# Optimization experiments

Hardware: AMD Instinct MI355X
Metric: run time of the kernel (lower is better)

Reference implementation:

```python
import jax, jax.numpy as jnp
import numpy as np

DIST_W = 1.0
LOGIT_W = 1.0


def _lsa(cost):
    """Rectangular linear sum assignment (Jonker-Volgenant shortest augmenting
    path), numpy-vectorized inner loop. cost: (n, m) with n <= m.
    Returns (row_ind, col_ind) matching scipy.optimize.linear_sum_assignment."""
    cost = np.asarray(cost, dtype=np.float64)
    n, m = cost.shape
    assert n <= m
    INF = 1e18
    u = np.zeros(n + 1)
    v = np.zeros(m + 1)
    p = np.zeros(m + 1, dtype=np.int64)   # p[j] = row matched to col j (1-based), 0 = free
    way = np.zeros(m + 1, dtype=np.int64)
    for i in range(1, n + 1):
        p[0] = i
        j0 = 0
        minv = np.full(m + 1, INF)
        used = np.zeros(m + 1, dtype=bool)
        while True:
            used[j0] = True
            i0 = p[j0]
            js = np.nonzero(~used[1:])[0] + 1          # free columns (1-based)
            cur = cost[i0 - 1, js - 1] - u[i0] - v[js]
            better = cur < minv[js]
            minv[js] = np.where(better, cur, minv[js])
            way[js[better]] = j0
            k = int(np.argmin(minv[js]))
            delta = minv[js][k]
            j1 = int(js[k])
            u[p[used]] += delta
            v[used] -= delta
            minv[~used] -= delta
            j0 = j1
            if p[j0] == 0:
                break
        # augment along the alternating path
        while j0 != 0:
            j1 = way[j0]
            p[j0] = p[j1]
            j0 = j1
    row_ind = np.arange(n, dtype=np.int64)
    col_ind = np.zeros(n, dtype=np.int64)
    for j in range(1, m + 1):
        if p[j] > 0:
            col_ind[p[j] - 1] = j - 1
    return row_ind, col_ind


def _cost_matrices(coordinates_gt, coordinates_pred, logits_gt, logits_pred):
    # Euclidean cdist (N, M) over D=2 coords
    d = coordinates_gt[:, None, :] - coordinates_pred[None, :, :]
    cost_distance = jnp.sqrt(jnp.sum(d * d, axis=-1))
    cost_matrix = cost_distance * DIST_W
    if LOGIT_W > 0:
        # L1 cdist (N, M) over L logits; [N, M, L] broadcast is the big intermediate
        cost_logits = jnp.sum(jnp.abs(logits_gt[:, None, :] - logits_pred[None, :, :]), axis=-1)
        cost_matrix = cost_matrix + cost_logits * LOGIT_W
    return cost_distance, cost_matrix


def setup_inputs() -> dict:
    key = jax.random.key(0)
    k1, k2, k3, k4 = jax.random.split(key, 4)
    return {
        "coordinates_gt": jax.random.uniform(k1, (256, 2), dtype=jnp.float32),
        "coordinates_pred": jax.random.uniform(k2, (1024, 2), dtype=jnp.float32),
        "logits_gt": jax.random.normal(k3, (256, 91), dtype=jnp.float32),
        "logits_pred": jax.random.normal(k4, (1024, 91), dtype=jnp.float32),
    }


def reference(coordinates_gt, coordinates_pred, logits_gt, logits_pred):
    cost_distance, cost_matrix = _cost_matrices(
        coordinates_gt, coordinates_pred, logits_gt, logits_pred)
    row, col = _lsa(np.asarray(jax.device_get(cost_matrix)))
    row = jnp.asarray(row)
    col = jnp.asarray(col)
    cost = cost_distance[row, col].sum()
    return (row, col, cost)
```

## Files before the change

kernel.cpp:

```cpp
#include <hip/hip_runtime.h>
#include <math.h>

#define N_GT 256
#define M_PR 1024
#define LG   91
#define TPB  256
#define CPT  4

#define DPPMIN(red, CTRL, RM, BM) do { \
    int _rh = __double2hiint(red), _rl = __double2loint(red); \
    int _oh = __builtin_amdgcn_update_dpp(_rh, _rh, CTRL, RM, BM, false); \
    int _ol = __builtin_amdgcn_update_dpp(_rl, _rl, CTRL, RM, BM, false); \
    (red) = fmin((red), __hiloint2double(_oh, _ol)); \
} while (0)

template<int F64>
__global__ __launch_bounds__(256) void cost_kernel(
    const float* __restrict__ cgt, const float* __restrict__ cpred,
    const float* __restrict__ lgt, const float* __restrict__ lpred,
    void* __restrict__ costout, float* __restrict__ rowmin, int* __restrict__ rowarg)
{
    __shared__ float sg[LG];
    __shared__ float gx, gy;
    __shared__ float wmin[4];
    __shared__ int   warg[4];
    const int i   = blockIdx.x;
    const int tid = threadIdx.x;
    if (tid < LG) sg[tid] = lgt[i * LG + tid];
    if (tid == 0) { gx = cgt[2 * i]; gy = cgt[2 * i + 1]; }
    __syncthreads();
    float bv = 1e30f; int bj = 0;
    for (int j = tid; j < M_PR; j += 256) {
        float dx = gx - cpred[2 * j];
        float dy = gy - cpred[2 * j + 1];
        float cd = sqrtf(dx * dx + dy * dy);
        const float* lp = lpred + j * LG;
        float s = 0.f;
        #pragma unroll 7
        for (int l = 0; l < LG; ++l) s += fabsf(sg[l] - lp[l]);
        float cv = cd + s;
        if (F64) ((double*)costout)[(size_t)i * M_PR + j] = (double)cv;
        else     ((float*) costout)[(size_t)i * M_PR + j] = cv;
        if (cv < bv) { bv = cv; bj = j; }
    }
    const int lane = tid & 63, wid = tid >> 6;
    #pragma unroll
    for (int off = 1; off < 64; off <<= 1) {
        float ov = __shfl_xor(bv, off, 64);
        int   oj = __shfl_xor(bj, off, 64);
        if (ov < bv || (ov == bv && oj < bj)) { bv = ov; bj = oj; }
    }
    if (lane == 0) { wmin[wid] = bv; warg[wid] = bj; }
    __syncthreads();
    if (tid == 0) {
        for (int w = 1; w < 4; ++w)
            if (wmin[w] < bv || (wmin[w] == bv && warg[w] < bj)) { bv = wmin[w]; bj = warg[w]; }
        rowmin[i] = bv; rowarg[i] = bj;
    }
}

template<int F64>
__global__ __launch_bounds__(256) void lsa_kernel(
    const void* __restrict__ costv,
    const float* __restrict__ rowmin, const int* __restrict__ rowarg,
    const float* __restrict__ cgt, const float* __restrict__ cpred,
    float* __restrict__ out)
{
    __shared__ double u[N_GT + 1];
    __shared__ double markD_lds[M_PR + 1];
    __shared__ double vsave_lds[M_PR + 1];
    __shared__ int    p[M_PR + 1];
    __shared__ int    pmin[M_PR + 1];
    __shared__ int    way[M_PR + 1];
    __shared__ int    pathbuf[N_GT + 8];
    __shared__ int    pathlen_s;
    __shared__ int    freeA[N_GT];
    __shared__ int    colarr[N_GT];
    __shared__ double2 wb[2][4];
    __shared__ int    wcnt[4];

    const int tid  = threadIdx.x;
    const int lane = tid & 63;
    const int wid  = tid >> 6;
    const double NEGINF = -__builtin_inf();
    const double INFD   =  __builtin_inf();

    double v[CPT], A[CPT];
    int    bw[CPT];

    const int colbase = tid * CPT;

    for (int j = tid; j <= M_PR; j += TPB) { p[j] = 0; pmin[j] = 0x7FFFFFFF; }
    colarr[tid] = 0;
    if (tid == 0) u[0] = 0.0;
    #pragma unroll
    for (int k = 0; k < CPT; ++k) { v[k] = 0.0; bw[k] = 0; }
    __syncthreads();

    u[tid + 1] = (double)rowmin[tid];
    atomicMin(&pmin[rowarg[tid] + 1], tid + 1);
    __syncthreads();
    for (int j = tid + 1; j <= M_PR; j += TPB)
        p[j] = (pmin[j] == 0x7FFFFFFF) ? 0 : pmin[j];
    {
        bool um = (pmin[rowarg[tid] + 1] != tid + 1);
        unsigned long long mask = __ballot(um);
        int local = __popcll(mask & ((1ull << lane) - 1ull));
        if (lane == 0) wcnt[wid] = __popcll(mask);
        __syncthreads();
        int base = 0;
        for (int w = 0; w < wid; ++w) base += wcnt[w];
        if (um) freeA[base + local] = tid + 1;
        __syncthreads();
    }
    const int nfree = wcnt[0] + wcnt[1] + wcnt[2] + wcnt[3];

    if (nfree > 0) {
        int nr = freeA[0];
        if (F64) {
            const double* nrow = (const double*)costv + (size_t)(nr - 1) * M_PR + colbase;
            double t0 = nrow[0];
            asm volatile("" :: "v"(t0));
        } else {
            const float* nrow = (const float*)costv + (size_t)(nr - 1) * M_PR + colbase;
            float t0 = nrow[0];
            asm volatile("" :: "v"(t0));
        }
    }

    int par = 0;
    for (int t = 0; t < nfree; ++t) {
        const int i = freeA[t];
        #pragma unroll
        for (int k = 0; k < CPT; ++k) A[k] = 1e18;
        unsigned usedmask = 0u;
        double D  = 0.0;
        int    j0 = 0;
        int    i0 = i;
        while (true) {
            double cd[CPT];
            if (F64) {
                const double2* rp = (const double2*)((const double*)costv
                                    + (size_t)(i0 - 1) * M_PR + colbase);
                double2 t0v = rp[0], t1v = rp[1];
                cd[0] = t0v.x; cd[1] = t0v.y; cd[2] = t1v.x; cd[3] = t1v.y;
            } else {
                const float4* rp = (const float4*)((const float*)costv
                                   + (size_t)(i0 - 1) * M_PR + colbase);
                float4 tv = rp[0];
                cd[0] = (double)tv.x; cd[1] = (double)tv.y;
                cd[2] = (double)tv.z; cd[3] = (double)tv.w;
            }
            double ui = u[i0];

            if (j0 > 0 && ((j0 - 1) >> 2) == tid) {
                const int okk = (j0 - 1) & 3;
                markD_lds[j0] = D;
                #pragma unroll
                for (int k = 0; k < CPT; ++k) {
                    if (k == okk) {
                        vsave_lds[j0] = v[k];
                        v[k] = NEGINF;
                        A[k] = INFD;
                        usedmask |= (1u << k);
                    }
                }
            }

            double   bAo  = INFD;
            unsigned bcwo = 0xFFFFFFFFu;
            #pragma unroll
            for (int k = 0; k < CPT; ++k) {
                unsigned cwk = ((unsigned)(colbase + k + 1) << 11) | (unsigned)bw[k];
                bool tk = A[k] < bAo;
                bAo  = tk ? A[k] : bAo;
                bcwo = tk ? cwk  : bcwo;
            }

            double base2 = ui - D;
            double vb[CPT];
            #pragma unroll
            for (int k = 0; k < CPT; ++k) vb[k] = v[k] + base2;

            double bAc = INFD; int bkc = 0;
            #pragma unroll
            for (int k = 0; k < CPT; ++k) {
                double cur = cd[k] - vb[k];
                bool upd = (cur < A[k]);
                A[k]  = upd ? cur : A[k];
                bw[k] = upd ? j0  : bw[k];
                bool tk = upd && (cur < bAc);
                bAc = tk ? cur : bAc;
                bkc = tk ? k   : bkc;
            }
            int      colc = colbase + bkc + 1;
            unsigned cwc  = ((unsigned)colc << 11) | (unsigned)j0;
            int      colo = (int)(bcwo >> 11);
            bool tc = (bAc < bAo) || (bAc == bAo && colc < colo);
            double   bA  = tc ? bAc : bAo;
            unsigned bcw = tc ? cwc : bcwo;

            int mycol = (int)(bcw >> 11);
            int pf = p[(mycol > M_PR) ? 0 : mycol];

            double red = bA;
            DPPMIN(red, 0x111, 0xf, 0xf);
            DPPMIN(red, 0x112, 0xf, 0xf);
            DPPMIN(red, 0x114, 0xf, 0xe);
            DPPMIN(red, 0x118, 0xf, 0xc);
            DPPMIN(red, 0x142, 0xa, 0xf);
            DPPMIN(red, 0x143, 0xc, 0xf);
            double Dw = __hiloint2double(
                __builtin_amdgcn_readlane(__double2hiint(red), 63),
                __builtin_amdgcn_readlane(__double2loint(red), 63));
            unsigned long long mm = __ballot(bA == Dw);
            int wl = __builtin_ctzll(mm);
            unsigned rcw = (unsigned)__builtin_amdgcn_readlane((int)bcw, wl);
            int      pfw = __builtin_amdgcn_readlane(pf, wl);
            if (lane == 0) {
                double2 rec;
                rec.x = Dw;
                rec.y = __hiloint2double((int)rcw, (int)pfw);
                wb[par][wid] = rec;
            }
            __syncthreads();
            double   bv_ = INFD;
            unsigned mcw = 0xFFFFFFFFu;
            int      mpf = 0;
            #pragma unroll
            for (int w = 0; w < 4; ++w) {
                double2 r = wb[par][w];
                unsigned rw  = (unsigned)__double2hiint(r.y);
                int      rpf = __double2loint(r.y);
                int      rcol = (int)(rw >> 11);
                bool b = (r.x < bv_) || (r.x == bv_ && rcol < (int)(mcw >> 11));
                bv_ = b ? r.x : bv_;
                mcw = b ? rw  : mcw;
                mpf = b ? rpf : mpf;
            }
            par ^= 1;
            D = bv_;
            int j1 = (int)(mcw >> 11);
            if (tid == 0) way[j1] = (int)(mcw & 2047u);
            j0 = j1;
            if (mpf == 0) break;
            i0 = mpf;
        }
        if (tid == 0) u[i] += D;
        #pragma unroll
        for (int k = 0; k < CPT; ++k) {
            if ((usedmask >> k) & 1u) {
                const int col = colbase + k + 1;
                double adj = D - markD_lds[col];
                v[k] = vsave_lds[col] - adj;
                int r = p[col];
                u[r] += adj;
            }
        }
        __syncthreads();
        if (tid == 0) {
            int L = 0, jj = j0;
            while (jj != 0) { pathbuf[L++] = jj; jj = way[jj]; }
            pathlen_s = L;
        }
        if (t + 1 < nfree) {
            int nr = freeA[t + 1];
            if (F64) {
                const double* nrow = (const double*)costv + (size_t)(nr - 1) * M_PR + colbase;
                double t0v = nrow[0];
                asm volatile("" :: "v"(t0v));
            } else {
                const float* nrow = (const float*)costv + (size_t)(nr - 1) * M_PR + colbase;
                float t0v = nrow[0];
                asm volatile("" :: "v"(t0v));
            }
        }
        __syncthreads();
        const int L = pathlen_s;
        int d0 = -1, s0 = 0, d1 = -1, s1 = 0;
        { int tt = tid;       if (tt < L) { d0 = pathbuf[tt]; s0 = (tt == L-1) ? i : p[pathbuf[tt+1]]; } }
        { int tt = tid + 256; if (tt < L) { d1 = pathbuf[tt]; s1 = (tt == L-1) ? i : p[pathbuf[tt+1]]; } }
        __syncthreads();
        if (d0 >= 0) p[d0] = s0;
        if (d1 >= 0) p[d1] = s1;
        __syncthreads();
    }

    #pragma unroll
    for (int k = 0; k < CPT; ++k) {
        int j  = colbase + k + 1;
        int pr = p[j];
        if (pr > 0) colarr[pr - 1] = j - 1;
    }
    __syncthreads();

    out[tid]        = (float)tid;
    out[N_GT + tid] = (float)colarr[tid];
    if (tid < 64) {
        float s = 0.f;
        for (int idx = lane; idx < N_GT; idx += 64) {
            int c = colarr[idx];
            c = (c < 0) ? 0 : (c >= M_PR ? M_PR - 1 : c);
            float dx = cgt[2 * idx]     - cpred[2 * c];
            float dy = cgt[2 * idx + 1] - cpred[2 * c + 1];
            s += sqrtf(dx * dx + dy * dy);
        }
        #pragma unroll
        for (int off = 1; off < 64; off <<= 1) s += __shfl_xor(s, off, 64);
        if (lane == 0) out[2 * N_GT] = s;
    }
}

extern "C" void kernel_launch(void* const* d_in, const int* in_sizes, int n_in,
                              void* d_out, int out_size, void* d_ws, size_t ws_size,
                              hipStream_t stream)
{
    const float* cgt   = (const float*)d_in[0];
    const float* cpred = (const float*)d_in[1];
    const float* lgt   = (const float*)d_in[2];
    const float* lpred = (const float*)d_in[3];
    float* out  = (float*)d_out;

    char* ws = (char*)d_ws;
    const size_t mat64 = (size_t)N_GT * M_PR * 8;
    const size_t mat32 = (size_t)N_GT * M_PR * 4;

    if (ws_size >= mat64 + 4096) {
        void*  cost   = (void*)ws;
        float* rowmin = (float*)(ws + mat64);
        int*   rowarg = (int*)  (ws + mat64 + 1024);
        cost_kernel<1><<<N_GT, 256, 0, stream>>>(cgt, cpred, lgt, lpred, cost, rowmin, rowarg);
        lsa_kernel<1><<<1, 256, 0, stream>>>(cost, rowmin, rowarg, cgt, cpred, out);
    } else {
        void*  cost   = (void*)ws;
        float* rowmin = (float*)(ws + mat32);
        int*   rowarg = (int*)  (ws + mat32 + 1024);
        cost_kernel<0><<<N_GT, 256, 0, stream>>>(cgt, cpred, lgt, lpred, cost, rowmin, rowarg);
        lsa_kernel<0><<<1, 256, 0, stream>>>(cost, rowmin, rowarg, cgt, cpred, out);
    }
}
```

Measured before the change: 283.1 us.

## Speculatively prefetch all four wave candidates' cost rows before selecting the winner

After the cross-wave barrier, every thread loads the cost-row slices and dual u values for all four per-wave candidate rows at once. It then chooses among them with a tree reduction and selects the matching data without branching. The intent is to take the dependent global load of the next row off the serial augmenting-path critical path by issuing the loads in parallel with the final min selection. The cost is four times the memory traffic per iteration, more register pressure, and the removal of the old single-row warmup prefetch.

```diff
diff --git a/kernel.cpp b/kernel.cpp
--- a/kernel.cpp
+++ b/kernel.cpp
@@ -115,19 +115,6 @@
     }
     const int nfree = wcnt[0] + wcnt[1] + wcnt[2] + wcnt[3];
 
-    if (nfree > 0) {
-        int nr = freeA[0];
-        if (F64) {
-            const double* nrow = (const double*)costv + (size_t)(nr - 1) * M_PR + colbase;
-            double t0 = nrow[0];
-            asm volatile("" :: "v"(t0));
-        } else {
-            const float* nrow = (const float*)costv + (size_t)(nr - 1) * M_PR + colbase;
-            float t0 = nrow[0];
-            asm volatile("" :: "v"(t0));
-        }
-    }
-
     int par = 0;
     for (int t = 0; t < nfree; ++t) {
         const int i = freeA[t];
@@ -136,23 +123,23 @@
         unsigned usedmask = 0u;
         double D  = 0.0;
         int    j0 = 0;
-        int    i0 = i;
+
+        double cd[CPT];
+        if (F64) {
+            const double2* rp = (const double2*)((const double*)costv
+                                + (size_t)(i - 1) * M_PR + colbase);
+            double2 t0v = rp[0], t1v = rp[1];
+            cd[0] = t0v.x; cd[1] = t0v.y; cd[2] = t1v.x; cd[3] = t1v.y;
+        } else {
+            const float4* rp = (const float4*)((const float*)costv
+                               + (size_t)(i - 1) * M_PR + colbase);
+            float4 tv = rp[0];
+            cd[0] = (double)tv.x; cd[1] = (double)tv.y;
+            cd[2] = (double)tv.z; cd[3] = (double)tv.w;
+        }
+        double ui = u[i];
+
         while (true) {
-            double cd[CPT];
-            if (F64) {
-                const double2* rp = (const double2*)((const double*)costv
-                                    + (size_t)(i0 - 1) * M_PR + colbase);
-                double2 t0v = rp[0], t1v = rp[1];
-                cd[0] = t0v.x; cd[1] = t0v.y; cd[2] = t1v.x; cd[3] = t1v.y;
-            } else {
-                const float4* rp = (const float4*)((const float*)costv
-                                   + (size_t)(i0 - 1) * M_PR + colbase);
-                float4 tv = rp[0];
-                cd[0] = (double)tv.x; cd[1] = (double)tv.y;
-                cd[2] = (double)tv.z; cd[3] = (double)tv.w;
-            }
-            double ui = u[i0];
-
             if (j0 > 0 && ((j0 - 1) >> 2) == tid) {
                 const int okk = (j0 - 1) & 3;
                 markD_lds[j0] = D;
@@ -224,27 +211,76 @@
                 wb[par][wid] = rec;
             }
             __syncthreads();
-            double   bv_ = INFD;
-            unsigned mcw = 0xFFFFFFFFu;
-            int      mpf = 0;
-            #pragma unroll
-            for (int w = 0; w < 4; ++w) {
-                double2 r = wb[par][w];
-                unsigned rw  = (unsigned)__double2hiint(r.y);
-                int      rpf = __double2loint(r.y);
-                int      rcol = (int)(rw >> 11);
-                bool b = (r.x < bv_) || (r.x == bv_ && rcol < (int)(mcw >> 11));
-                bv_ = b ? r.x : bv_;
-                mcw = b ? rw  : mcw;
-                mpf = b ? rpf : mpf;
-            }
+            double2 r0 = wb[par][0], r1 = wb[par][1];
+            double2 r2 = wb[par][2], r3 = wb[par][3];
             par ^= 1;
-            D = bv_;
+            int rp0 = __double2loint(r0.y), rp1 = __double2loint(r1.y);
+            int rp2 = __double2loint(r2.y), rp3 = __double2loint(r3.y);
+
+            double n0[CPT], n1[CPT], n2[CPT], n3[CPT];
+            if (F64) {
+                const double* base = (const double*)costv;
+                const double2* q0 = (const double2*)(base + (size_t)((rp0 > 0 ? rp0 : 1) - 1) * M_PR + colbase);
+                const double2* q1 = (const double2*)(base + (size_t)((rp1 > 0 ? rp1 : 1) - 1) * M_PR + colbase);
+                const double2* q2 = (const double2*)(base + (size_t)((rp2 > 0 ? rp2 : 1) - 1) * M_PR + colbase);
+                const double2* q3 = (const double2*)(base + (size_t)((rp3 > 0 ? rp3 : 1) - 1) * M_PR + colbase);
+                double2 a0 = q0[0], b0 = q0[1];
+                double2 a1 = q1[0], b1 = q1[1];
+                double2 a2 = q2[0], b2 = q2[1];
+                double2 a3 = q3[0], b3 = q3[1];
+                n0[0]=a0.x; n0[1]=a0.y; n0[2]=b0.x; n0[3]=b0.y;
+                n1[0]=a1.x; n1[1]=a1.y; n1[2]=b1.x; n1[3]=b1.y;
+                n2[0]=a2.x; n2[1]=a2.y; n2[2]=b2.x; n2[3]=b2.y;
+                n3[0]=a3.x; n3[1]=a3.y; n3[2]=b3.x; n3[3]=b3.y;
+            } else {
+                const float* base = (const float*)costv;
+                float4 a0 = *(const float4*)(base + (size_t)((rp0 > 0 ? rp0 : 1) - 1) * M_PR + colbase);
+                float4 a1 = *(const float4*)(base + (size_t)((rp1 > 0 ? rp1 : 1) - 1) * M_PR + colbase);
+                float4 a2 = *(const float4*)(base + (size_t)((rp2 > 0 ? rp2 : 1) - 1) * M_PR + colbase);
+                float4 a3 = *(const float4*)(base + (size_t)((rp3 > 0 ? rp3 : 1) - 1) * M_PR + colbase);
+                n0[0]=(double)a0.x; n0[1]=(double)a0.y; n0[2]=(double)a0.z; n0[3]=(double)a0.w;
+                n1[0]=(double)a1.x; n1[1]=(double)a1.y; n1[2]=(double)a1.z; n1[3]=(double)a1.w;
+                n2[0]=(double)a2.x; n2[1]=(double)a2.y; n2[2]=(double)a2.z; n2[3]=(double)a2.w;
+                n3[0]=(double)a3.x; n3[1]=(double)a3.y; n3[2]=(double)a3.z; n3[3]=(double)a3.w;
+            }
+            double u0 = u[rp0 > 0 ? rp0 : 0], u1 = u[rp1 > 0 ? rp1 : 0];
+            double u2 = u[rp2 > 0 ? rp2 : 0], u3 = u[rp3 > 0 ? rp3 : 0];
+
+            unsigned c0 = (unsigned)__double2hiint(r0.y), c1 = (unsigned)__double2hiint(r1.y);
+            unsigned c2 = (unsigned)__double2hiint(r2.y), c3 = (unsigned)__double2hiint(r3.y);
+            bool b01 = (r1.x < r0.x) || (r1.x == r0.x && (c1 >> 11) < (c0 >> 11));
+            double   v01 = b01 ? r1.x : r0.x;
+            unsigned w01 = b01 ? c1   : c0;
+            int      p01 = b01 ? rp1  : rp0;
+            int      s01 = b01 ? 1    : 0;
+            bool b23 = (r3.x < r2.x) || (r3.x == r2.x && (c3 >> 11) < (c2 >> 11));
+            double   v23 = b23 ? r3.x : r2.x;
+            unsigned w23 = b23 ? c3   : c2;
+            int      p23 = b23 ? rp3  : rp2;
+            int      s23 = b23 ? 3    : 2;
+            bool bf = (v23 < v01) || (v23 == v01 && (w23 >> 11) < (w01 >> 11));
+            D            = bf ? v23 : v01;
+            unsigned mcw = bf ? w23 : w01;
+            int      mpf = bf ? p23 : p01;
+            int      wsel = bf ? s23 : s01;
+
             int j1 = (int)(mcw >> 11);
             if (tid == 0) way[j1] = (int)(mcw & 2047u);
             j0 = j1;
             if (mpf == 0) break;
-            i0 = mpf;
+
+            const bool ws1 = (wsel & 1) != 0, ws2 = (wsel & 2) != 0;
+            #pragma unroll
+            for (int k = 0; k < CPT; ++k) {
+                double e01 = ws1 ? n1[k] : n0[k];
+                double e23 = ws1 ? n3[k] : n2[k];
+                cd[k] = ws2 ? e23 : e01;
+            }
+            {
+                double e01 = ws1 ? u1 : u0;
+                double e23 = ws1 ? u3 : u2;
+                ui = ws2 ? e23 : e01;
+            }
         }
         if (tid == 0) u[i] += D;
         #pragma unroll
```

New measurement: 314.5 us. 11.1% more time.
